# Kernel tuning notes

Hardware: AMD Instinct MI355X
Metric: run time of the kernel (lower is better)

The kernel has to match this reference:

```python
import jax, jax.numpy as jnp
import numpy as np
import math

B, T, D_MODEL, N_HEADS = 4, 2048, 1024, 16
D_HEAD = D_MODEL // N_HEADS


def _rope_freqs(t, d_head):
    inv = 1.0 / (10000.0 ** (np.arange(0, d_head, 2, dtype=np.float32) / d_head))
    ang = np.arange(t, dtype=np.float32)[:, None] * inv[None, :]  # (T, d_head//2)
    return jnp.asarray(np.cos(ang)), jnp.asarray(np.sin(ang))


def setup_inputs() -> dict:
    key = jax.random.key(0)
    k1, k2, k3, k4, k5 = jax.random.split(key, 5)
    s = 1.0 / math.sqrt(D_MODEL)
    x = jax.random.normal(k1, (B, T, D_MODEL), dtype=jnp.float32)
    mask = jnp.triu(jnp.ones((T, T), dtype=bool), k=1)  # causal: mask future positions
    freqs_cos, freqs_sin = _rope_freqs(T, D_HEAD)
    qkv_w = jax.random.uniform(k2, (3 * D_MODEL, D_MODEL), jnp.float32, -s, s)
    qkv_b = jax.random.uniform(k3, (3 * D_MODEL,), jnp.float32, -s, s)
    proj_w = jax.random.uniform(k4, (D_MODEL, D_MODEL), jnp.float32, -s, s)
    proj_b = jax.random.uniform(k5, (D_MODEL,), jnp.float32, -s, s)
    return {"x": x, "mask": mask, "freqs_cos": freqs_cos, "freqs_sin": freqs_sin,
            "qkv_w": qkv_w, "qkv_b": qkv_b, "proj_w": proj_w, "proj_b": proj_b}


def _apply_rope(t, cos, sin):
    # t: (B, H, T, D_HEAD); cos/sin: (T, D_HEAD//2), broadcast over B, H
    tp = t.reshape(*t.shape[:-1], -1, 2)
    a, b = tp[..., 0], tp[..., 1]
    out_r = a * cos - b * sin
    out_i = a * sin + b * cos
    return jnp.stack([out_r, out_i], axis=-1).reshape(t.shape)


def reference(x, mask, freqs_cos, freqs_sin, qkv_w, qkv_b, proj_w, proj_b):
    Bx, Tx, C = x.shape
    qkv = x @ qkv_w.T + qkv_b  # (B, T, 3C)
    q, k, v = jnp.split(qkv, 3, axis=-1)
    def heads(z):
        return z.reshape(Bx, Tx, N_HEADS, D_HEAD).transpose(0, 2, 1, 3)  # (B,H,T,dh)
    q, k, v = heads(q), heads(k), heads(v)
    q = _apply_rope(q, freqs_cos, freqs_sin)
    k = _apply_rope(k, freqs_cos, freqs_sin)
    att = jnp.einsum('bhqd,bhkd->bhqk', q, k) / math.sqrt(D_HEAD)
    att = jnp.where(mask, -jnp.inf, att)
    att = jax.nn.softmax(att, axis=-1)
    out = jnp.einsum('bhqk,bhkd->bhqd', att, v)
    out = out.transpose(0, 2, 1, 3).reshape(Bx, Tx, C)
    return out @ proj_w.T + proj_b
```

## Files before the change

kernel.cpp:

```cpp
#include <hip/hip_runtime.h>
#include <stdint.h>

#define BB 4
#define TT 2048
#define CC 1024
#define HH 16
#define DH 64
#define NQKV 3072

typedef __bf16 bf16_t;
typedef __attribute__((ext_vector_type(8))) __bf16 bf16x8;
typedef __attribute__((ext_vector_type(4))) __bf16 bf16x4;
typedef __attribute__((ext_vector_type(4))) float f32x4;

#define MFMA16(a, b, c) __builtin_amdgcn_mfma_f32_16x16x32_bf16((a), (b), (c), 0, 0, 0)

__device__ __forceinline__ void gll16(const void* g, void* l) {
  typedef const __attribute__((address_space(1))) void* gp_t;
  typedef __attribute__((address_space(3))) void* lp_t;
  __builtin_amdgcn_global_load_lds((gp_t)(uintptr_t)g, (lp_t)(uintptr_t)l, 16, 0, 0);
}

__global__ __launch_bounds__(256) void cvt_k(const float* __restrict__ src,
                                             bf16_t* __restrict__ dst, int n) {
  const int i8 = (blockIdx.x * 256 + threadIdx.x) * 8;
  if (i8 < n) {
    const f32x4 a = *(const f32x4*)(src + i8);
    const f32x4 b = *(const f32x4*)(src + i8 + 4);
    bf16x8 r;
    r[0] = (bf16_t)a[0]; r[1] = (bf16_t)a[1]; r[2] = (bf16_t)a[2]; r[3] = (bf16_t)a[3];
    r[4] = (bf16_t)b[0]; r[5] = (bf16_t)b[1]; r[6] = (bf16_t)b[2]; r[7] = (bf16_t)b[3];
    *(bf16x8*)(dst + i8) = r;
  }
}

__global__ __launch_bounds__(256) void cvt2_k(const float* __restrict__ s0,
                                              bf16_t* __restrict__ d0, int n0,
                                              const float* __restrict__ s1,
                                              bf16_t* __restrict__ d1, int n1) {
  const int i8 = (blockIdx.x * 256 + threadIdx.x) * 8;
  const float* src;
  bf16_t* dst;
  if (i8 < n0) {
    src = s0 + i8;
    dst = d0 + i8;
  } else {
    const int k = i8 - n0;
    if (k >= n1) return;
    src = s1 + k;
    dst = d1 + k;
  }
  const f32x4 a = *(const f32x4*)(src);
  const f32x4 b = *(const f32x4*)(src + 4);
  bf16x8 r;
  r[0] = (bf16_t)a[0]; r[1] = (bf16_t)a[1]; r[2] = (bf16_t)a[2]; r[3] = (bf16_t)a[3];
  r[4] = (bf16_t)b[0]; r[5] = (bf16_t)b[1]; r[6] = (bf16_t)b[2]; r[7] = (bf16_t)b[3];
  *(bf16x8*)dst = r;
}

template <int EPI>
__global__ __launch_bounds__(256) void gemm_k(
    const bf16_t* __restrict__ A, const bf16_t* __restrict__ W,
    const float* __restrict__ bias,
    const float* __restrict__ fcos, const float* __restrict__ fsin,
    void* __restrict__ out0v, bf16_t* __restrict__ out1,
    bf16_t* __restrict__ out2) {
  __shared__ bf16_t Alds[2][128 * 32];
  __shared__ bf16_t Blds[2][128 * 32];
  const int K = 1024;
  const int tid = threadIdx.x;
  const int lane = tid & 63, wave = tid >> 6;
  const int quad = lane >> 4, c = lane & 15;
  const int wm = wave >> 1, wn = wave & 1;

  const int nx = gridDim.x;
  const int d = blockIdx.y * nx + blockIdx.x;
  const int cpx = (nx * gridDim.y) >> 3;
  const int xcd = d & 7, j = d >> 3;
  const int nyl = cpx / nx;
  const int stpr = nx >> 2;
  const int st = j >> 4, wi = j & 15;
  const int bx = (st % stpr) * 4 + (wi & 3);
  const int by = xcd * nyl + (st / stpr) * 4 + (wi >> 2);
  const int mbase = by * 128, nbase = bx * 128;

  f32x4 acc[4][4];
#pragma unroll
  for (int i = 0; i < 4; ++i)
#pragma unroll
    for (int j2 = 0; j2 < 4; ++j2) acc[i][j2] = (f32x4){0.f, 0.f, 0.f, 0.f};

  const int s0 = tid, s1 = tid + 256;
  const int r0 = s0 >> 2, cc0 = (s0 & 3) ^ (r0 & 3);
  const int r1 = s1 >> 2, cc1 = (s1 & 3) ^ (r1 & 3);
  const bf16_t* ag0 = A + (mbase + r0) * K + cc0 * 8;
  const bf16_t* ag1 = A + (mbase + r1) * K + cc1 * 8;
  const bf16_t* bg0 = W + (nbase + r0) * K + cc0 * 8;
  const bf16_t* bg1 = W + (nbase + r1) * K + cc1 * 8;

#define GSTAGE(BUF, KO)                        \
  {                                            \
    gll16(ag0 + (KO), &Alds[BUF][s0 * 8]);     \
    gll16(ag1 + (KO), &Alds[BUF][s1 * 8]);     \
    gll16(bg0 + (KO), &Blds[BUF][s0 * 8]);     \
    gll16(bg1 + (KO), &Blds[BUF][s1 * 8]);     \
  }

#define GSTEP(KS, CUR, STG)                                                    \
  {                                                                            \
    if (STG) GSTAGE((CUR) ^ 1, ((KS) + 1) * 32);                               \
    bf16x8 af[4], bfr[4];                                                      \
    _Pragma("unroll") for (int mi = 0; mi < 4; ++mi) {                         \
      const int row = wm * 64 + mi * 16 + c;                                   \
      af[mi] = *(const bf16x8*)&Alds[CUR][(row * 4 + (quad ^ (row & 3))) * 8]; \
    }                                                                          \
    _Pragma("unroll") for (int ni = 0; ni < 4; ++ni) {                         \
      const int row = wn * 64 + ni * 16 + c;                                   \
      bfr[ni] =                                                                \
          *(const bf16x8*)&Blds[CUR][(row * 4 + (quad ^ (row & 3))) * 8];      \
    }                                                                          \
    _Pragma("unroll") for (int mi = 0; mi < 4; ++mi)                           \
        _Pragma("unroll") for (int ni = 0; ni < 4; ++ni)                       \
            acc[mi][ni] = MFMA16(af[mi], bfr[ni], acc[mi][ni]);                \
    if (STG) {                                                                 \
      asm volatile("s_waitcnt vmcnt(0)" ::: "memory");                         \
      __builtin_amdgcn_s_barrier();                                            \
      asm volatile("" ::: "memory");                                           \
    }                                                                          \
  }

  GSTAGE(0, 0);
  asm volatile("s_waitcnt vmcnt(0)" ::: "memory");
  __builtin_amdgcn_s_barrier();
  asm volatile("" ::: "memory");

  for (int fj = 0; fj < 15; ++fj) {
    GSTEP(2 * fj, 0, 1)
    GSTEP(2 * fj + 1, 1, 1)
  }
  GSTEP(30, 0, 1)
  GSTEP(31, 1, 0)
#undef GSTEP
#undef GSTAGE

  const float qscale = 0.18033688011112042f;
#pragma unroll
  for (int mi = 0; mi < 4; ++mi) {
#pragma unroll
    for (int ni = 0; ni < 4; ++ni) {
      const int n = nbase + wn * 64 + ni * 16 + c;
      const float bv = bias[n];
#pragma unroll
      for (int r = 0; r < 4; ++r) {
        const int m = mbase + wm * 64 + mi * 16 + quad * 4 + r;
        float v = acc[mi][ni][r] + bv;
        if (EPI == 0) {
          bf16_t* out0 = (bf16_t*)out0v;
          const int sel = n >> 10;
          const int nl = n & 1023;
          const int h = nl >> 6, dd = nl & 63;
          const int b = m >> 11, t = m & 2047;
          const int dst = ((b * HH + h) * TT + t) * DH + dd;
          if (sel < 2) {
            const float pv = __shfl_xor(v, 1, 64);
            const int d2 = dd >> 1;
            const float cs = fcos[t * 32 + d2];
            const float sn = fsin[t * 32 + d2];
            float o = ((dd & 1) == 0) ? (v * cs - pv * sn) : (pv * sn + v * cs);
            if (sel == 0) {
              o *= qscale;
              out0[dst] = (bf16_t)o;
            } else {
              out1[dst] = (bf16_t)o;
            }
          } else {
            out2[dst] = (bf16_t)v;
          }
        } else {
          float* outf = (float*)out0v;
          outf[m * CC + n] = v;
        }
      }
    }
  }
}

__global__ __launch_bounds__(256, 4) void attn_k(const bf16_t* __restrict__ Q,
                                                 const bf16_t* __restrict__ Kv,
                                                 const bf16_t* __restrict__ V,
                                                 bf16_t* __restrict__ O) {
  __shared__ bf16_t KS[2][64 * 64];
  __shared__ bf16_t VtS[2][64 * 64];
  __shared__ bf16_t PS[4][16 * 64];

  const int tid = threadIdx.x;
  const int lane = tid & 63, wave = tid >> 6;
  const int quad = lane >> 4, c = lane & 15;
  const int d0 = blockIdx.x;
  const int bi = (d0 & 7) * 128 + (d0 >> 3);
  const int pair = bi & 15, h = (bi >> 4) & 15, b = bi >> 8;
  const int qtA = pair, qtB = 31 - pair;
  const int nA = qtA + 1;

  const bf16_t* Qh = Q + ((b * HH + h) * TT) * DH;
  const bf16_t* Kh = Kv + ((b * HH + h) * TT) * DH;
  const bf16_t* Vh = V + ((b * HH + h) * TT) * DH;

  const f32x4 zero4 = {0.f, 0.f, 0.f, 0.f};
  bf16x8 ones8;
#pragma unroll
  for (int i = 0; i < 8; ++i) ones8[i] = (bf16_t)1.0f;

  const int krow0 = tid >> 3, kc8 = tid & 7, krow1 = krow0 + 32;
  const bf16_t* kbase0 = Kh + krow0 * DH + kc8 * 8;
  const bf16_t* kbase1 = Kh + krow1 * DH + kc8 * 8;
  const int vsb = tid >> 2, vjp = tid & 3;
  const int vrg = vsb & 7, vc8 = vsb >> 3;
  const int vd0 = vc8 * 8 + vjp * 2, vd1 = vd0 + 1;
  const bf16_t* vbase = Vh + vrg * 8 * DH + vd0;

  const int sw = c & 7;
  const int e0 = c * 64 + (quad ^ sw) * 8;
  const int e1 = c * 64 + ((quad + 4) ^ sw) * 8;

  bf16x8 kr0, kr1;
  uint32_t vr[8];
  auto load_tile = [&](int eoff) {
    kr0 = *(const bf16x8*)(kbase0 + eoff);
    kr1 = *(const bf16x8*)(kbase1 + eoff);
    const bf16_t* vp = vbase + eoff;
#pragma unroll
    for (int i = 0; i < 8; ++i) vr[i] = *(const uint32_t*)(vp + i * DH);
  };
  auto store_tile = [&](int buf) {
    *(bf16x8*)&KS[buf][(krow0 * 8 + (kc8 ^ (krow0 & 7))) * 8] = kr0;
    *(bf16x8*)&KS[buf][(krow1 * 8 + (kc8 ^ (krow1 & 7))) * 8] = kr1;
    union { bf16x8 v; uint16_t u[8]; } colA, colB;
#pragma unroll
    for (int i = 0; i < 8; ++i) {
      colA.u[i] = (uint16_t)(vr[i] & 0xffffu);
      colB.u[i] = (uint16_t)(vr[i] >> 16);
    }
    *(bf16x8*)&VtS[buf][(vd0 * 8 + (vrg ^ (vd0 & 7))) * 8] = colA.v;
    *(bf16x8*)&VtS[buf][(vd1 * 8 + (vrg ^ (vd1 & 7))) * 8] = colB.v;
  };

  int qtbase = qtA * 64;
  bf16x8 qf0 = *(const bf16x8*)(Qh + (qtbase + wave * 16 + c) * DH + quad * 8);
  bf16x8 qf1 = *(const bf16x8*)(Qh + (qtbase + wave * 16 + c) * DH + 32 + quad * 8);

  f32x4 o_acc[4] = {zero4, zero4, zero4, zero4};
  float m_s = -1e30f;
  float l_r[4] = {0.f, 0.f, 0.f, 0.f};

  auto write_O = [&](int qtb) {
#pragma unroll
    for (int r = 0; r < 4; ++r) {
      const int qg = qtb + wave * 16 + quad * 4 + r;
      const float inv = 1.0f / l_r[r];
#pragma unroll
      for (int ni = 0; ni < 4; ++ni)
        O[(b * TT + qg) * CC + h * 64 + ni * 16 + c] =
            (bf16_t)(o_acc[ni][r] * inv);
    }
  };

  load_tile(0);
  store_tile(0);
  __syncthreads();
  int coff = 0;
  int kkey = 0;

#define ATTN_ITER(FI, CUR)                                                     \
  {                                                                            \
    const int fi_ = (FI);                                                      \
    const bool pre_ = fi_ < 32;                                                \
    const int noff_ = (fi_ + 1 == nA) ? 0 : coff + 64 * DH;                    \
    if (pre_) load_tile(noff_);                                                \
    bf16x8 kf0[4], kf1[4];                                                     \
    _Pragma("unroll") for (int ni = 0; ni < 4; ++ni) {                         \
      kf0[ni] = *(const bf16x8*)&KS[CUR][ni * 1024 + e0];                      \
      kf1[ni] = *(const bf16x8*)&KS[CUR][ni * 1024 + e1];                      \
    }                                                                          \
    \
    f32x4 s[4];                                                                \
    _Pragma("unroll") for (int ni = 0; ni < 4; ++ni) {                         \
      f32x4 t = MFMA16(kf0[ni], qf0, zero4);                                   \
      t = MFMA16(kf1[ni], qf1, t);                                             \
      s[ni] = t;                                                               \
    }                                                                          \
    const int minq_ = qtbase + wave * 16;                                      \
    if (kkey + 63 > minq_) {                                                   \
      const int qg_ = minq_ + c;                                               \
      _Pragma("unroll") for (int ni = 0; ni < 4; ++ni)                         \
          _Pragma("unroll") for (int r = 0; r < 4; ++r) {                      \
        const int key_ = kkey + ni * 16 + quad * 4 + r;                        \
        if (key_ > qg_) s[ni][r] = -1e30f;                                     \
      }                                                                        \
    }                                                                          \
                      \
    float a0_ = fmaxf(fmaxf(s[0][0], s[0][1]), fmaxf(s[0][2], s[0][3]));       \
    float a1_ = fmaxf(fmaxf(s[1][0], s[1][1]), fmaxf(s[1][2], s[1][3]));       \
    float a2_ = fmaxf(fmaxf(s[2][0], s[2][1]), fmaxf(s[2][2], s[2][3]));       \
    float a3_ = fmaxf(fmaxf(s[3][0], s[3][1]), fmaxf(s[3][2], s[3][3]));       \
    float mx = fmaxf(fmaxf(a0_, a1_), fmaxf(a2_, a3_));                        \
    mx = fmaxf(mx, __shfl_xor(mx, 16, 64));                                    \
    mx = fmaxf(mx, __shfl_xor(mx, 32, 64));                                    \
                 \
    if (__any(mx > m_s + 8.0f)) {                                              \
      const float mnew = fmaxf(m_s, mx);                                       \
      const float al = __builtin_amdgcn_exp2f(m_s - mnew);                     \
      m_s = mnew;                                                              \
      _Pragma("unroll") for (int r = 0; r < 4; ++r) {                          \
        const float alD = __shfl(al, (lane & 48) | (quad * 4 + r), 64);        \
        l_r[r] *= alD;                                                         \
        _Pragma("unroll") for (int ni = 0; ni < 4; ++ni)                       \
            o_acc[ni][r] *= alD;                                               \
      }                                                                        \
    }                                                                          \
         \
    _Pragma("unroll") for (int ni = 0; ni < 4; ++ni) {                         \
      bf16x4 pk_;                                                              \
      _Pragma("unroll") for (int r = 0; r < 4; ++r)                            \
          pk_[r] = (bf16_t)__builtin_amdgcn_exp2f(s[ni][r] - m_s);             \
      *(bf16x4*)&PS[wave][(c * 8 + ((2 * ni + (quad >> 1)) ^ sw)) * 8 +        \
                          (quad & 1) * 4] = pk_;                               \
    }                                                                          \
    asm volatile("s_waitcnt lgkmcnt(0)" ::: "memory");                         \
    const bf16x8 p0 = *(const bf16x8*)&PS[wave][e0];                           \
    const bf16x8 p1 = *(const bf16x8*)&PS[wave][e1];                           \
    f32x4 rs = MFMA16(p0, ones8, zero4);                                       \
    rs = MFMA16(p1, ones8, rs);                                                \
    _Pragma("unroll") for (int ni = 0; ni < 4; ++ni) {                         \
      const bf16x8 v0 = *(const bf16x8*)&VtS[CUR][ni * 1024 + e0];             \
      const bf16x8 v1 = *(const bf16x8*)&VtS[CUR][ni * 1024 + e1];             \
      o_acc[ni] = MFMA16(p0, v0, o_acc[ni]);                                   \
      o_acc[ni] = MFMA16(p1, v1, o_acc[ni]);                                   \
    }                                                                          \
    _Pragma("unroll") for (int r = 0; r < 4; ++r) l_r[r] += rs[r];             \
    if (fi_ == nA - 1) {                                                       \
      write_O(qtbase);                                                         \
      qtbase = qtB * 64;                                                       \
      qf0 = *(const bf16x8*)(Qh + (qtbase + wave * 16 + c) * DH + quad * 8);   \
      qf1 = *(const bf16x8*)(Qh + (qtbase + wave * 16 + c) * DH + 32 +         \
                             quad * 8);                                        \
      m_s = -1e30f;                                                            \
      _Pragma("unroll") for (int r = 0; r < 4; ++r) l_r[r] = 0.f;              \
      _Pragma("unroll") for (int ni = 0; ni < 4; ++ni) o_acc[ni] = zero4;      \
    }                                                                          \
    if (pre_) store_tile(1 - (CUR));                                           \
    __syncthreads();                                                           \
    coff = noff_;                                                              \
    kkey = (fi_ + 1 == nA) ? 0 : kkey + 64;                                    \
  }

  for (int fj = 0; fj < 16; ++fj) {
    ATTN_ITER(2 * fj, 0)
    ATTN_ITER(2 * fj + 1, 1)
  }
  ATTN_ITER(32, 0)
#undef ATTN_ITER

  write_O(qtbase);
}

extern "C" void kernel_launch(void* const* d_in, const int* in_sizes, int n_in,
                              void* d_out, int out_size, void* d_ws,
                              size_t ws_size, hipStream_t stream) {
  const float *x = nullptr, *fcos = nullptr, *fsin = nullptr;
  const float *qkv_w = nullptr, *qkv_b = nullptr, *proj_w = nullptr, *proj_b = nullptr;
  for (int i = 0; i < n_in; ++i) {
    const int s = in_sizes[i];
    const float* p = (const float*)d_in[i];
    if (s == BB * TT * CC) x = p;
    else if (s == TT * (DH / 2)) { if (!fcos) fcos = p; else fsin = p; }
    else if (s == NQKV * CC) qkv_w = p;
    else if (s == NQKV) qkv_b = p;
    else if (s == CC * CC) proj_w = p;
    else if (s == CC) proj_b = p;
  }

  const size_t NE = (size_t)BB * TT * CC;
  bf16_t* Qb = (bf16_t*)d_ws;
  bf16_t* Kb = Qb + NE;
  bf16_t* Vb = Kb + NE;
  bf16_t* Ob = Vb + NE;
  bf16_t* xb = Ob;
  bf16_t* wqkvb = (bf16_t*)d_out;
  bf16_t* wpb = Qb;

  const int n0 = (int)NE, n1 = NQKV * CC;
  cvt2_k<<<dim3((n0 + n1) / 2048), 256, 0, stream>>>(x, xb, n0, qkv_w, wqkvb,
                                                     n1);

  gemm_k<0><<<dim3(NQKV / 128, (BB * TT) / 128), 256, 0, stream>>>(
      xb, wqkvb, qkv_b, fcos, fsin, (void*)Qb, Kb, Vb);
  attn_k<<<dim3(BB * HH * 16), 256, 0, stream>>>(Qb, Kb, Vb, Ob);
  cvt_k<<<dim3(CC * CC / 2048), 256, 0, stream>>>(proj_w, wpb, CC * CC);
  gemm_k<1><<<dim3(CC / 128, (BB * TT) / 128), 256, 0, stream>>>(
      Ob, wpb, proj_b, nullptr, nullptr, d_out, nullptr, nullptr);
}
```

Before: 278.2 us.

## Make QKV GEMM persistent over two tiles and fold proj weight conversion

The QKV GEMM now runs half as many blocks, each processing two output tiles in sequence. It prefetches the first K-slab of the next tile before running the current tile's epilogue, so the RoPE/store epilogue overlaps the next tile's loads. When the workspace is large enough, the projection weight conversion is merged into the initial conversion kernel, which removes one launch. The cost is fewer concurrently resident blocks for the QKV GEMM (768 vs 1536 tiles over 256 CUs), which may change wave quantization and load balance.

```diff
diff --git a/kernel.cpp b/kernel.cpp
--- a/kernel.cpp
+++ b/kernel.cpp
@@ -21,35 +21,7 @@
   __builtin_amdgcn_global_load_lds((gp_t)(uintptr_t)g, (lp_t)(uintptr_t)l, 16, 0, 0);
 }
 
-__global__ __launch_bounds__(256) void cvt_k(const float* __restrict__ src,
-                                             bf16_t* __restrict__ dst, int n) {
-  const int i8 = (blockIdx.x * 256 + threadIdx.x) * 8;
-  if (i8 < n) {
-    const f32x4 a = *(const f32x4*)(src + i8);
-    const f32x4 b = *(const f32x4*)(src + i8 + 4);
-    bf16x8 r;
-    r[0] = (bf16_t)a[0]; r[1] = (bf16_t)a[1]; r[2] = (bf16_t)a[2]; r[3] = (bf16_t)a[3];
-    r[4] = (bf16_t)b[0]; r[5] = (bf16_t)b[1]; r[6] = (bf16_t)b[2]; r[7] = (bf16_t)b[3];
-    *(bf16x8*)(dst + i8) = r;
-  }
-}
-
-__global__ __launch_bounds__(256) void cvt2_k(const float* __restrict__ s0,
-                                              bf16_t* __restrict__ d0, int n0,
-                                              const float* __restrict__ s1,
-                                              bf16_t* __restrict__ d1, int n1) {
-  const int i8 = (blockIdx.x * 256 + threadIdx.x) * 8;
-  const float* src;
-  bf16_t* dst;
-  if (i8 < n0) {
-    src = s0 + i8;
-    dst = d0 + i8;
-  } else {
-    const int k = i8 - n0;
-    if (k >= n1) return;
-    src = s1 + k;
-    dst = d1 + k;
-  }
+__device__ __forceinline__ void cvt8(const float* src, bf16_t* dst) {
   const f32x4 a = *(const f32x4*)(src);
   const f32x4 b = *(const f32x4*)(src + 4);
   bf16x8 r;
@@ -58,7 +30,35 @@
   *(bf16x8*)dst = r;
 }
 
-template <int EPI>
+__global__ __launch_bounds__(256) void cvt_k(const float* __restrict__ src,
+                                             bf16_t* __restrict__ dst, int n) {
+  const int i8 = (blockIdx.x * 256 + threadIdx.x) * 8;
+  if (i8 < n) cvt8(src + i8, dst + i8);
+}
+
+__global__ __launch_bounds__(256) void cvt2_k(const float* __restrict__ s0,
+                                              bf16_t* __restrict__ d0, int n0,
+                                              const float* __restrict__ s1,
+                                              bf16_t* __restrict__ d1, int n1) {
+  int i8 = (blockIdx.x * 256 + threadIdx.x) * 8;
+  if (i8 < n0) { cvt8(s0 + i8, d0 + i8); return; }
+  i8 -= n0;
+  if (i8 < n1) cvt8(s1 + i8, d1 + i8);
+}
+
+__global__ __launch_bounds__(256) void cvt3_k(
+    const float* __restrict__ s0, bf16_t* __restrict__ d0, int n0,
+    const float* __restrict__ s1, bf16_t* __restrict__ d1, int n1,
+    const float* __restrict__ s2, bf16_t* __restrict__ d2, int n2) {
+  int i8 = (blockIdx.x * 256 + threadIdx.x) * 8;
+  if (i8 < n0) { cvt8(s0 + i8, d0 + i8); return; }
+  i8 -= n0;
+  if (i8 < n1) { cvt8(s1 + i8, d1 + i8); return; }
+  i8 -= n1;
+  if (i8 < n2) cvt8(s2 + i8, d2 + i8);
+}
+
+template <int EPI, int NT>
 __global__ __launch_bounds__(256) void gemm_k(
     const bf16_t* __restrict__ A, const bf16_t* __restrict__ W,
     const float* __restrict__ bias,
@@ -74,29 +74,36 @@
   const int wm = wave >> 1, wn = wave & 1;
 
   const int nx = gridDim.x;
-  const int d = blockIdx.y * nx + blockIdx.x;
-  const int cpx = (nx * gridDim.y) >> 3;
-  const int xcd = d & 7, j = d >> 3;
+  const int pstep = nx * gridDim.y;
+  const int nlog = pstep * NT;
+  const int cpx = nlog >> 3;
   const int nyl = cpx / nx;
   const int stpr = nx >> 2;
-  const int st = j >> 4, wi = j & 15;
-  const int bx = (st % stpr) * 4 + (wi & 3);
-  const int by = xcd * nyl + (st / stpr) * 4 + (wi >> 2);
-  const int mbase = by * 128, nbase = bx * 128;
-
-  f32x4 acc[4][4];
-#pragma unroll
-  for (int i = 0; i < 4; ++i)
-#pragma unroll
-    for (int j2 = 0; j2 < 4; ++j2) acc[i][j2] = (f32x4){0.f, 0.f, 0.f, 0.f};
+  const int pbase = blockIdx.y * nx + blockIdx.x;
+
+  auto remap = [&](int dd, int& mb, int& nb) {
+    const int xcd = dd & 7, j = dd >> 3;
+    const int st = j >> 4, wi = j & 15;
+    const int bx = (st % stpr) * 4 + (wi & 3);
+    const int by = xcd * nyl + (st / stpr) * 4 + (wi >> 2);
+    mb = by * 128;
+    nb = bx * 128;
+  };
+
+  int mbase, nbase;
+  remap(pbase, mbase, nbase);
 
   const int s0 = tid, s1 = tid + 256;
   const int r0 = s0 >> 2, cc0 = (s0 & 3) ^ (r0 & 3);
   const int r1 = s1 >> 2, cc1 = (s1 & 3) ^ (r1 & 3);
-  const bf16_t* ag0 = A + (mbase + r0) * K + cc0 * 8;
-  const bf16_t* ag1 = A + (mbase + r1) * K + cc1 * 8;
-  const bf16_t* bg0 = W + (nbase + r0) * K + cc0 * 8;
-  const bf16_t* bg1 = W + (nbase + r1) * K + cc1 * 8;
+  const bf16_t *ag0, *ag1, *bg0, *bg1;
+  auto setptrs = [&]() {
+    ag0 = A + (mbase + r0) * K + cc0 * 8;
+    ag1 = A + (mbase + r1) * K + cc1 * 8;
+    bg0 = W + (nbase + r0) * K + cc0 * 8;
+    bg1 = W + (nbase + r1) * K + cc1 * 8;
+  };
+  setptrs();
 
 #define GSTAGE(BUF, KO)                        \
   {                                            \
@@ -134,55 +141,82 @@
   __builtin_amdgcn_s_barrier();
   asm volatile("" ::: "memory");
 
-  for (int fj = 0; fj < 15; ++fj) {
-    GSTEP(2 * fj, 0, 1)
-    GSTEP(2 * fj + 1, 1, 1)
-  }
-  GSTEP(30, 0, 1)
-  GSTEP(31, 1, 0)
+  const float qscale = 0.18033688011112042f;
+
+  for (int tt = 0; tt < NT; ++tt) {
+    f32x4 acc[4][4];
+#pragma unroll
+    for (int i = 0; i < 4; ++i)
+#pragma unroll
+      for (int j2 = 0; j2 < 4; ++j2) acc[i][j2] = (f32x4){0.f, 0.f, 0.f, 0.f};
+
+    for (int fj = 0; fj < 15; ++fj) {
+      GSTEP(2 * fj, 0, 1)
+      GSTEP(2 * fj + 1, 1, 1)
+    }
+    GSTEP(30, 0, 1)
+    GSTEP(31, 1, 0)
+
+    int mb2 = 0, nb2 = 0;
+    if (tt + 1 < NT) {
+      remap(pbase + (tt + 1) * pstep, mb2, nb2);
+      const int msave = mbase, nsave = nbase;
+      mbase = mb2; nbase = nb2;
+      setptrs();
+      GSTAGE(0, 0);
+      mbase = msave; nbase = nsave;
+    }
+
+#pragma unroll
+    for (int mi = 0; mi < 4; ++mi) {
+#pragma unroll
+      for (int ni = 0; ni < 4; ++ni) {
+        const int n = nbase + wn * 64 + ni * 16 + c;
+        const float bv = bias[n];
+#pragma unroll
+        for (int r = 0; r < 4; ++r) {
+          const int m = mbase + wm * 64 + mi * 16 + quad * 4 + r;
+          float v = acc[mi][ni][r] + bv;
+          if (EPI == 0) {
+            bf16_t* out0 = (bf16_t*)out0v;
+            const int sel = n >> 10;
+            const int nl = n & 1023;
+            const int h = nl >> 6, dd = nl & 63;
+            const int b = m >> 11, t = m & 2047;
+            const int dst = ((b * HH + h) * TT + t) * DH + dd;
+            if (sel < 2) {
+              const float pv = __shfl_xor(v, 1, 64);
+              const int d2 = dd >> 1;
+              const float cs = fcos[t * 32 + d2];
+              const float sn = fsin[t * 32 + d2];
+              float o = ((dd & 1) == 0) ? (v * cs - pv * sn) : (pv * sn + v * cs);
+              if (sel == 0) {
+                o *= qscale;
+                out0[dst] = (bf16_t)o;
+              } else {
+                out1[dst] = (bf16_t)o;
+              }
+            } else {
+              out2[dst] = (bf16_t)v;
+            }
+          } else {
+            float* outf = (float*)out0v;
+            outf[m * CC + n] = v;
+          }
+        }
+      }
+    }
+
+    if (tt + 1 < NT) {
+      mbase = mb2; nbase = nb2;
+      setptrs();
+      asm volatile("s_waitcnt vmcnt(0)" ::: "memory");
+      __builtin_amdgcn_s_barrier();
+      asm volatile("" ::: "memory");
+    }
+  }
 #undef GSTEP
 #undef GSTAGE
-
-  const float qscale = 0.18033688011112042f;
-#pragma unroll
-  for (int mi = 0; mi < 4; ++mi) {
-#pragma unroll
-    for (int ni = 0; ni < 4; ++ni) {
-      const int n = nbase + wn * 64 + ni * 16 + c;
-      const float bv = bias[n];
-#pragma unroll
-      for (int r = 0; r < 4; ++r) {
-        const int m = mbase + wm * 64 + mi * 16 + quad * 4 + r;
-        float v = acc[mi][ni][r] + bv;
-        if (EPI == 0) {
-          bf16_t* out0 = (bf16_t*)out0v;
-          const int sel = n >> 10;
-          const int nl = n & 1023;
-          const int h = nl >> 6, dd = nl & 63;
-          const int b = m >> 11, t = m & 2047;
-          const int dst = ((b * HH + h) * TT + t) * DH + dd;
-          if (sel < 2) {
-            const float pv = __shfl_xor(v, 1, 64);
-            const int d2 = dd >> 1;
-            const float cs = fcos[t * 32 + d2];
-            const float sn = fsin[t * 32 + d2];
-            float o = ((dd & 1) == 0) ? (v * cs - pv * sn) : (pv * sn + v * cs);
-            if (sel == 0) {
-              o *= qscale;
-              out0[dst] = (bf16_t)o;
-            } else {
-              out1[dst] = (bf16_t)o;
-            }
-          } else {
-            out2[dst] = (bf16_t)v;
-          }
-        } else {
-          float* outf = (float*)out0v;
-          outf[m * CC + n] = v;
-        }
-      }
-    }
-  }
 }
 
 __global__ __launch_bounds__(256, 4) void attn_k(const bf16_t* __restrict__ Q,
@@ -387,16 +421,25 @@
   bf16_t* Ob = Vb + NE;
   bf16_t* xb = Ob;
   bf16_t* wqkvb = (bf16_t*)d_out;
-  bf16_t* wpb = Qb;
-
-  const int n0 = (int)NE, n1 = NQKV * CC;
-  cvt2_k<<<dim3((n0 + n1) / 2048), 256, 0, stream>>>(x, xb, n0, qkv_w, wqkvb,
-                                                     n1);
-
-  gemm_k<0><<<dim3(NQKV / 128, (BB * TT) / 128), 256, 0, stream>>>(
+
+  const int n0 = (int)NE, n1 = NQKV * CC, n2 = CC * CC;
+  const bool bigws = ws_size >= (size_t)(4 * NE + (size_t)n2) * sizeof(bf16_t);
+  bf16_t* wpb = bigws ? (Ob + NE) : Qb;
+
+  if (bigws) {
+    cvt3_k<<<dim3((n0 + n1 + n2) / 2048), 256, 0, stream>>>(
+        x, xb, n0, qkv_w, wqkvb, n1, proj_w, wpb, n2);
+  } else {
+    cvt2_k<<<dim3((n0 + n1) / 2048), 256, 0, stream>>>(x, xb, n0, qkv_w, wqkvb,
+                                                       n1);
+  }
+
+  gemm_k<0, 2><<<dim3(NQKV / 128, (BB * TT) / 256), 256, 0, stream>>>(
       xb, wqkvb, qkv_b, fcos, fsin, (void*)Qb, Kb, Vb);
   attn_k<<<dim3(BB * HH * 16), 256, 0, stream>>>(Qb, Kb, Vb, Ob);
-  cvt_k<<<dim3(CC * CC / 2048), 256, 0, stream>>>(proj_w, wpb, CC * CC);
-  gemm_k<1><<<dim3(CC / 128, (BB * TT) / 128), 256, 0, stream>>>(
+  if (!bigws) {
+    cvt_k<<<dim3(n2 / 2048), 256, 0, stream>>>(proj_w, wpb, n2);
+  }
+  gemm_k<1, 1><<<dim3(CC / 128, (BB * TT) / 128), 256, 0, stream>>>(
       Ob, wpb, proj_b, nullptr, nullptr, d_out, nullptr, nullptr);
 }
```

Result: slower. 297.2 us (+6.8%).
